# Kernel tuning notes

Hardware: AMD Instinct MI355X
Metric: run time of the kernel (lower is better)

## Reference

```python
import jax, jax.numpy as jnp
import numpy as np

B, S, H = 512, 200, 256

def setup_inputs() -> dict:
    key = jax.random.key(0)
    ks = jax.random.split(key, 7)
    scale = 1.0 / np.sqrt(H)
    return {
        "all_memory": jax.random.normal(ks[0], (B, S, H), dtype=jnp.float32),
        "last_memory": jax.random.normal(ks[1], (B, H), dtype=jnp.float32),
        "U": jax.random.normal(ks[2], (H, H), dtype=jnp.float32) * scale,   # U_meta weight
        "W": jax.random.normal(ks[3], (H, H), dtype=jnp.float32) * scale,   # W_meta weight
        "V": jax.random.normal(ks[4], (H, 1), dtype=jnp.float32) * scale,   # V_meta weight (stored as [H,1])
        "MetaW": jax.random.normal(ks[5], (4, H), dtype=jnp.float32) * scale,  # Meta weight
        "Metab": jax.random.normal(ks[6], (4,), dtype=jnp.float32) * scale,    # Meta bias ('multiple' mode)
    }

def reference(all_memory, last_memory, U, W, V, MetaW, Metab):
    # U_meta(all_memory): [B,S,H]; W_meta(last_memory): [B,H] broadcast over S
    a = jnp.einsum('bsh,kh->bsk', all_memory, U)
    l = jnp.einsum('bh,kh->bk', last_memory, W)
    # additive attention score: V_meta(tanh(a + l)) -> [B,S]
    scores = jnp.einsum('bsh,h->bs', jnp.tanh(a + l[:, None, :]), V[:, 0])
    alpha = jax.nn.softmax(scores, axis=1)  # softmax over seq dim
    pooled = jnp.einsum('bs,bsh->bh', alpha, all_memory)  # weighted sum of values
    return pooled @ MetaW.T + Metab  # [B, 4]
```

## Files before the change

### kernel.cpp

```cpp
#include <hip/hip_runtime.h>
#include <hip/hip_bf16.h>
#include <math.h>

#define NB 512
#define NS 200
#define NH 256
#define TILE_S 32
#define LDSPAD 8
#define LDW (NH + LDSPAD)
#define WS_STRIDE 258
#define NPART (NB * 2)

#define OFF_PART 0
#define OFF_L    (NPART * WS_STRIDE)
#define OFF_UB   (OFF_L + NB * NH)
#define WS_FLOATS_PRE  (OFF_UB + (NH * NH) / 2)

typedef _Float16 f16x8 __attribute__((ext_vector_type(8)));
typedef float    f32x4 __attribute__((ext_vector_type(4)));

__global__ __launch_bounds__(256)
void precompute(const float* __restrict__ lastm, const float* __restrict__ W,
                const float* __restrict__ U,
                float* __restrict__ l_ws, _Float16* __restrict__ Uswz)
{
  const int t = threadIdx.x;
  if (blockIdx.x < NB) {
    const int b = blockIdx.x;
    __shared__ float lm_sm[NH];
    lm_sm[t] = lastm[(size_t)b * NH + t];
    __syncthreads();
    const float4* wrow = (const float4*)(W + (size_t)t * NH);
    const float4* lrow = (const float4*)lm_sm;
    float a0 = 0.f, a1 = 0.f, a2 = 0.f, a3 = 0.f;
#pragma unroll 8
    for (int i = 0; i < NH / 4; ++i) {
      float4 w4 = wrow[i];
      float4 m4 = lrow[i];
      a0 = fmaf(w4.x, m4.x, a0);
      a1 = fmaf(w4.y, m4.y, a1);
      a2 = fmaf(w4.z, m4.z, a2);
      a3 = fmaf(w4.w, m4.w, a3);
    }
    l_ws[(size_t)b * NH + t] = (a0 + a1) + (a2 + a3);
  } else {
    const int id    = (blockIdx.x - NB) * 256 + t;
    const int n_blk = id >> 9;
    const int kk    = (id >> 6) & 7;
    const int lane  = id & 63;
    const int row   = n_blk * 16 + (lane & 15);
    const int col   = kk * 32 + (lane >> 4) * 8;
    const float4* s = (const float4*)(U + (size_t)row * NH + col);
    const float4 a = s[0], c = s[1];
    f16x8 pk;
    pk[0] = (_Float16)a.x; pk[1] = (_Float16)a.y;
    pk[2] = (_Float16)a.z; pk[3] = (_Float16)a.w;
    pk[4] = (_Float16)c.x; pk[5] = (_Float16)c.y;
    pk[6] = (_Float16)c.z; pk[7] = (_Float16)c.w;
    *(f16x8*)(Uswz + (size_t)id * 8) = pk;
  }
}

template<bool PRE>
__global__ __launch_bounds__(512, 4)
void fused_meta_attn_part(const float* __restrict__ mem,
                          const float* __restrict__ lastm,
                          const float* __restrict__ U,
                          const float* __restrict__ W,
                          const float* __restrict__ V,
                          const float* __restrict__ l_ws,
                          const _Float16* __restrict__ Uswz,
                          float* __restrict__ part)
{
  const int b    = blockIdx.x >> 1;
  const int half = blockIdx.x & 1;
  const int s_begin = half ? 96 : 0;
  const int s_end   = half ? NS : 96;
  const int ntiles  = half ? 4 : 3;

  const int t     = threadIdx.x;
  const int wave  = t >> 6;
  const int lane  = t & 63;
  const int m16   = lane & 15;
  const int quad  = lane >> 4;
  const int hcol  = t & 255;
  const int rhalf = t >> 8;

  __shared__ __align__(16) _Float16 hi_sm[TILE_S][LDW];
  __shared__ __align__(16) _Float16 lo_sm[TILE_S][LDW];
  __shared__ float swave_sm[8][TILE_S];
  __shared__ __align__(16) float e_sm[TILE_S];
  __shared__ float mz_sm[2];
  __shared__ float l_sm[NH];
  __shared__ float lm_sm[NH];

  if (!PRE) {
    if (t < NH) lm_sm[t] = lastm[(size_t)b * NH + t];
    __syncthreads();
    if (t < NH) {
      const float4* wrow = (const float4*)(W + (size_t)t * NH);
      const float4* lrow = (const float4*)lm_sm;
      float a0 = 0.f, a1 = 0.f, a2 = 0.f, a3 = 0.f;
#pragma unroll 8
      for (int i = 0; i < NH / 4; ++i) {
        float4 w4 = wrow[i];
        float4 m4 = lrow[i];
        a0 = fmaf(w4.x, m4.x, a0);
        a1 = fmaf(w4.y, m4.y, a1);
        a2 = fmaf(w4.z, m4.z, a2);
        a3 = fmaf(w4.w, m4.w, a3);
      }
      l_sm[t] = (a0 + a1) + (a2 + a3);
    }
    __syncthreads();
  }

  float l_reg[2], v_reg[2];
#pragma unroll
  for (int nf = 0; nf < 2; ++nf) {
    const int n = wave * 32 + nf * 16 + m16;
    l_reg[nf] = PRE ? l_ws[(size_t)b * NH + n] : l_sm[n];
    v_reg[nf] = V[n];
  }
  const float vsum  = v_reg[0] + v_reg[1];
  const float vm2_0 = -2.f * v_reg[0];
  const float vm2_1 = -2.f * v_reg[1];

  f16x8 u_frag[2][8];
  if (PRE) {
    const _Float16* uw = Uswz + ((size_t)(wave * 2 * 8 * 64) + lane) * 8;
#pragma unroll
    for (int nf = 0; nf < 2; ++nf)
#pragma unroll
      for (int kk = 0; kk < 8; ++kk)
        u_frag[nf][kk] = *(const f16x8*)(uw + (size_t)((nf * 8 + kk) << 9));
  } else {
#pragma unroll
    for (int nf = 0; nf < 2; ++nf) {
      const int n = wave * 32 + nf * 16 + m16;
      const float* urow = U + (size_t)n * NH;
#pragma unroll
      for (int kk = 0; kk < 8; ++kk) {
        const float4 lo = *(const float4*)(urow + kk * 32 + quad * 8);
        const float4 hi = *(const float4*)(urow + kk * 32 + quad * 8 + 4);
        f16x8 f;
        f[0] = (_Float16)lo.x; f[1] = (_Float16)lo.y;
        f[2] = (_Float16)lo.z; f[3] = (_Float16)lo.w;
        f[4] = (_Float16)hi.x; f[5] = (_Float16)hi.y;
        f[6] = (_Float16)hi.z; f[7] = (_Float16)hi.w;
        u_frag[nf][kk] = f;
      }
    }
  }

  float m_run  = -INFINITY;
  float Z      = 0.f;
  float pooled = 0.f;

  for (int tile = 0; tile < ntiles; ++tile) {
    const int s0   = s_begin + tile * TILE_S;
    const int rows = min(TILE_S, s_end - s0);

    const float4* src4 = (const float4*)(mem + ((size_t)b * NS + s0) * NH);
#pragma unroll
    for (int i = 0; i < 2; ++i) {
      const int f2  = i * 512 + t;
      const int row = f2 >> 5;
      const int c8  = (f2 & 31) * 8;
      f16x8 ph, pl;
      if (row < rows) {
        const float4 a = src4[f2 * 2];
        const float4 c = src4[f2 * 2 + 1];
#define CVT_HL(idx, val) { const float x_ = (val); const _Float16 h_ = (_Float16)x_; \
                           ph[idx] = h_; pl[idx] = (_Float16)(x_ - (float)h_); }
        CVT_HL(0, a.x) CVT_HL(1, a.y) CVT_HL(2, a.z) CVT_HL(3, a.w)
        CVT_HL(4, c.x) CVT_HL(5, c.y) CVT_HL(6, c.z) CVT_HL(7, c.w)
#undef CVT_HL
      } else {
        ph = (f16x8)(_Float16)0.f;
        pl = (f16x8)(_Float16)0.f;
      }
      *(f16x8*)&hi_sm[row][c8] = ph;
      *(f16x8*)&lo_sm[row][c8] = pl;
    }
    __syncthreads();

    f32x4 acc[2][2];
    const f32x4 fzero = {0.f, 0.f, 0.f, 0.f};
#pragma unroll
    for (int mt = 0; mt < 2; ++mt)
#pragma unroll
      for (int nf = 0; nf < 2; ++nf)
        acc[mt][nf] = fzero;

#pragma unroll
    for (int kk = 0; kk < 8; ++kk) {
      const int c = kk * 32 + quad * 8;
      f16x8 a0h = *(const f16x8*)&hi_sm[m16][c];
      f16x8 a1h = *(const f16x8*)&hi_sm[16 + m16][c];
      f16x8 a0l = *(const f16x8*)&lo_sm[m16][c];
      f16x8 a1l = *(const f16x8*)&lo_sm[16 + m16][c];
#pragma unroll
      for (int nf = 0; nf < 2; ++nf) {
        acc[0][nf] = __builtin_amdgcn_mfma_f32_16x16x32_f16(a0h, u_frag[nf][kk], acc[0][nf], 0, 0, 0);
        acc[1][nf] = __builtin_amdgcn_mfma_f32_16x16x32_f16(a1h, u_frag[nf][kk], acc[1][nf], 0, 0, 0);
        acc[0][nf] = __builtin_amdgcn_mfma_f32_16x16x32_f16(a0l, u_frag[nf][kk], acc[0][nf], 0, 0, 0);
        acc[1][nf] = __builtin_amdgcn_mfma_f32_16x16x32_f16(a1l, u_frag[nf][kk], acc[1][nf], 0, 0, 0);
      }
    }

    float p[2][4];
#pragma unroll
    for (int mt = 0; mt < 2; ++mt) {
#pragma unroll
      for (int reg = 0; reg < 4; ++reg) {
        const float x0 = acc[mt][0][reg] + l_reg[0];
        const float x1 = acc[mt][1][reg] + l_reg[1];
        const float e0 = __expf(x0 + x0);
        const float e1 = __expf(x1 + x1);
        float s = vsum;
        s += __fdividef(vm2_0, e0 + 1.f);
        s += __fdividef(vm2_1, e1 + 1.f);
        p[mt][reg] = s;
      }
    }
#pragma unroll
    for (int off = 1; off < 16; off <<= 1) {
#pragma unroll
      for (int mt = 0; mt < 2; ++mt)
#pragma unroll
        for (int reg = 0; reg < 4; ++reg)
          p[mt][reg] += __shfl_xor(p[mt][reg], off);
    }
    if (m16 == 0) {
#pragma unroll
      for (int mt = 0; mt < 2; ++mt)
#pragma unroll
        for (int reg = 0; reg < 4; ++reg)
          swave_sm[wave][mt * 16 + quad * 4 + reg] = p[mt][reg];
    }
    __syncthreads();

    if (t < TILE_S) {
      float s = swave_sm[0][t];
#pragma unroll
      for (int w = 1; w < 8; ++w) s += swave_sm[w][t];
      const float sv = (t < rows) ? s : -INFINITY;
      float mt_ = sv;
#pragma unroll
      for (int off = 1; off < 32; off <<= 1)
        mt_ = fmaxf(mt_, __shfl_xor(mt_, off));
      const float m_new = fmaxf(m_run, mt_);
      float e = (t < rows) ? __expf(sv - m_new) : 0.f;
      e_sm[t] = e;
      float z = e;
#pragma unroll
      for (int off = 1; off < 32; off <<= 1)
        z += __shfl_xor(z, off);
      if (t == 0) { mz_sm[0] = m_new; mz_sm[1] = z; }
    }
    __syncthreads();

    const float m_new = mz_sm[0];
    const float z_new = mz_sm[1];
    const float fac   = __expf(m_run - m_new);
    m_run = m_new;
    Z = fmaf(Z, fac, z_new);

    const int r0 = rhalf * 16;
    const float4 ev0 = *(const float4*)&e_sm[r0 + 0];
    const float4 ev1 = *(const float4*)&e_sm[r0 + 4];
    const float4 ev2 = *(const float4*)&e_sm[r0 + 8];
    const float4 ev3 = *(const float4*)&e_sm[r0 + 12];
    float pt = 0.f;
    pt = fmaf(ev0.x, (float)hi_sm[r0 +  0][hcol], pt);
    pt = fmaf(ev0.y, (float)hi_sm[r0 +  1][hcol], pt);
    pt = fmaf(ev0.z, (float)hi_sm[r0 +  2][hcol], pt);
    pt = fmaf(ev0.w, (float)hi_sm[r0 +  3][hcol], pt);
    pt = fmaf(ev1.x, (float)hi_sm[r0 +  4][hcol], pt);
    pt = fmaf(ev1.y, (float)hi_sm[r0 +  5][hcol], pt);
    pt = fmaf(ev1.z, (float)hi_sm[r0 +  6][hcol], pt);
    pt = fmaf(ev1.w, (float)hi_sm[r0 +  7][hcol], pt);
    pt = fmaf(ev2.x, (float)hi_sm[r0 +  8][hcol], pt);
    pt = fmaf(ev2.y, (float)hi_sm[r0 +  9][hcol], pt);
    pt = fmaf(ev2.z, (float)hi_sm[r0 + 10][hcol], pt);
    pt = fmaf(ev2.w, (float)hi_sm[r0 + 11][hcol], pt);
    pt = fmaf(ev3.x, (float)hi_sm[r0 + 12][hcol], pt);
    pt = fmaf(ev3.y, (float)hi_sm[r0 + 13][hcol], pt);
    pt = fmaf(ev3.z, (float)hi_sm[r0 + 14][hcol], pt);
    pt = fmaf(ev3.w, (float)hi_sm[r0 + 15][hcol], pt);
    pooled = fmaf(pooled, fac, pt);
    __syncthreads();
  }

  float* scratch = &swave_sm[0][0];
  if (rhalf == 1) scratch[hcol] = pooled;
  __syncthreads();
  float* base = part + (size_t)blockIdx.x * WS_STRIDE;
  if (t == 0) { base[0] = m_run; base[1] = Z; }
  if (rhalf == 0) base[2 + hcol] = pooled + scratch[hcol];
}

__global__ __launch_bounds__(256)
void merge_project(const float* __restrict__ part,
                   const float* __restrict__ MetaW,
                   const float* __restrict__ Metab,
                   float* __restrict__ out)
{
  const int b    = blockIdx.x;
  const int t    = threadIdx.x;
  const int wave = t >> 6;
  const int lane = t & 63;

  __shared__ float pooled_sm[NH];

  const float* b0 = part + (size_t)(b * 2)     * WS_STRIDE;
  const float* b1 = part + (size_t)(b * 2 + 1) * WS_STRIDE;
  const float m0 = b0[0], Z0 = b0[1];
  const float m1 = b1[0], Z1 = b1[1];
  const float mm = fmaxf(m0, m1);
  const float w0 = __expf(m0 - mm);
  const float w1 = __expf(m1 - mm);
  const float Zi = 1.f / (Z0 * w0 + Z1 * w1);

  pooled_sm[t] = (b0[2 + t] * w0 + b1[2 + t] * w1) * Zi;
  __syncthreads();

  float s = 0.f;
#pragma unroll
  for (int i = 0; i < 4; ++i) {
    const int h = i * 64 + lane;
    s = fmaf(pooled_sm[h], MetaW[(size_t)wave * NH + h], s);
  }
#pragma unroll
  for (int off = 32; off > 0; off >>= 1)
    s += __shfl_down(s, off);
  if (lane == 0)
    out[b * 4 + wave] = s + Metab[wave];
}

extern "C" void kernel_launch(void* const* d_in, const int* in_sizes, int n_in,
                              void* d_out, int out_size, void* d_ws, size_t ws_size,
                              hipStream_t stream) {
  const float* mem   = (const float*)d_in[0];
  const float* lastm = (const float*)d_in[1];
  const float* U     = (const float*)d_in[2];
  const float* W     = (const float*)d_in[3];
  const float* V     = (const float*)d_in[4];
  const float* MetaW = (const float*)d_in[5];
  const float* Metab = (const float*)d_in[6];
  float* out = (float*)d_out;
  float* ws  = (float*)d_ws;

  float* part = ws + OFF_PART;

  if (ws_size >= (size_t)WS_FLOATS_PRE * sizeof(float)) {
    float*    l_ws = ws + OFF_L;
    _Float16* Uswz = (_Float16*)(ws + OFF_UB);
    hipLaunchKernelGGL(precompute, dim3(NB + 32), dim3(256), 0, stream,
                       lastm, W, U, l_ws, Uswz);
    hipLaunchKernelGGL(fused_meta_attn_part<true>, dim3(NPART), dim3(512), 0, stream,
                       mem, lastm, U, W, V, l_ws, Uswz, part);
  } else {
    hipLaunchKernelGGL(fused_meta_attn_part<false>, dim3(NPART), dim3(512), 0, stream,
                       mem, lastm, U, W, V, (const float*)nullptr, (const _Float16*)nullptr, part);
  }
  hipLaunchKernelGGL(merge_project, dim3(NB), dim3(256), 0, stream,
                     part, MetaW, Metab, out);
}
```

Before: 210.8 us.

## Double-buffer memory tiles with register prefetch and use DPP row reductions

Stores the hi/lo fp16 memory tiles in two LDS buffers. The next tile is loaded from global into registers before the current tile's MFMA work and is converted and written to the other buffer during the softmax phase. This overlaps global loads with compute and removes one barrier per tile. It also swaps the shuffle-based 16-lane score reduction for DPP adds, and changes the pooled accumulation so each thread holds 8 columns over 2 rows, with a final 16-way LDS reduction. The larger LDS footprint may lower how many blocks fit per CU.

After: 246.7 us. 17.0% more time.

```diff
diff --git a/kernel.cpp b/kernel.cpp
--- a/kernel.cpp
+++ b/kernel.cpp
@@ -18,6 +18,19 @@
 
 typedef _Float16 f16x8 __attribute__((ext_vector_type(8)));
 typedef float    f32x4 __attribute__((ext_vector_type(4)));
+
+template<int CTRL>
+__device__ __forceinline__ float dpp_xadd(float v) {
+  return v + __int_as_float(
+      __builtin_amdgcn_update_dpp(0, __float_as_int(v), CTRL, 0xf, 0xf, true));
+}
+__device__ __forceinline__ float row16_sum(float v) {
+  v = dpp_xadd<0xB1>(v);
+  v = dpp_xadd<0x4E>(v);
+  v = dpp_xadd<0x124>(v);
+  v = dpp_xadd<0x128>(v);
+  return v;
+}
 
 __global__ __launch_bounds__(256)
 void precompute(const float* __restrict__ lastm, const float* __restrict__ W,
@@ -61,6 +74,9 @@
   }
 }
 
+#define CVT_HL(idx, val) { const float x_ = (val); const _Float16 h_ = (_Float16)x_; \
+                           ph[idx] = h_; pl[idx] = (_Float16)(x_ - (float)h_); }
+
 template<bool PRE>
 __global__ __launch_bounds__(512, 4)
 void fused_meta_attn_part(const float* __restrict__ mem,
@@ -83,18 +99,19 @@
   const int lane  = t & 63;
   const int m16   = lane & 15;
   const int quad  = lane >> 4;
-  const int hcol  = t & 255;
-  const int rhalf = t >> 8;
-
-  __shared__ __align__(16) _Float16 hi_sm[TILE_S][LDW];
-  __shared__ __align__(16) _Float16 lo_sm[TILE_S][LDW];
+  const int g     = t >> 5;
+  const int hblk  = (t & 31) * 8;
+
+  __shared__ __align__(16) _Float16 hi_sm[2][TILE_S][LDW];
+  __shared__ __align__(16) _Float16 lo_sm[2][TILE_S][LDW];
   __shared__ float swave_sm[8][TILE_S];
-  __shared__ __align__(16) float e_sm[TILE_S];
+  __shared__ float e_sm[TILE_S];
   __shared__ float mz_sm[2];
-  __shared__ float l_sm[NH];
-  __shared__ float lm_sm[NH];
-
-  if (!PRE) {
+
+  float l_reg[2], v_reg[2];
+  if constexpr (!PRE) {
+    __shared__ float l_sm[NH];
+    __shared__ float lm_sm[NH];
     if (t < NH) lm_sm[t] = lastm[(size_t)b * NH + t];
     __syncthreads();
     if (t < NH) {
@@ -113,21 +130,23 @@
       l_sm[t] = (a0 + a1) + (a2 + a3);
     }
     __syncthreads();
-  }
-
-  float l_reg[2], v_reg[2];
-#pragma unroll
-  for (int nf = 0; nf < 2; ++nf) {
-    const int n = wave * 32 + nf * 16 + m16;
-    l_reg[nf] = PRE ? l_ws[(size_t)b * NH + n] : l_sm[n];
-    v_reg[nf] = V[n];
-  }
+#pragma unroll
+    for (int nf = 0; nf < 2; ++nf)
+      l_reg[nf] = l_sm[wave * 32 + nf * 16 + m16];
+  } else {
+#pragma unroll
+    for (int nf = 0; nf < 2; ++nf)
+      l_reg[nf] = l_ws[(size_t)b * NH + wave * 32 + nf * 16 + m16];
+  }
+#pragma unroll
+  for (int nf = 0; nf < 2; ++nf)
+    v_reg[nf] = V[wave * 32 + nf * 16 + m16];
   const float vsum  = v_reg[0] + v_reg[1];
   const float vm2_0 = -2.f * v_reg[0];
   const float vm2_1 = -2.f * v_reg[1];
 
   f16x8 u_frag[2][8];
-  if (PRE) {
+  if constexpr (PRE) {
     const _Float16* uw = Uswz + ((size_t)(wave * 2 * 8 * 64) + lane) * 8;
 #pragma unroll
     for (int nf = 0; nf < 2; ++nf)
@@ -153,37 +172,49 @@
     }
   }
 
-  float m_run  = -INFINITY;
-  float Z      = 0.f;
-  float pooled = 0.f;
+  {
+    const float4* src4 = (const float4*)(mem + ((size_t)b * NS + s_begin) * NH);
+    const int f0 = t, f1 = 512 + t;
+    const float4 a0 = src4[f0 * 2], a1 = src4[f0 * 2 + 1];
+    const float4 b0 = src4[f1 * 2], b1 = src4[f1 * 2 + 1];
+    {
+      f16x8 ph, pl;
+      CVT_HL(0, a0.x) CVT_HL(1, a0.y) CVT_HL(2, a0.z) CVT_HL(3, a0.w)
+      CVT_HL(4, a1.x) CVT_HL(5, a1.y) CVT_HL(6, a1.z) CVT_HL(7, a1.w)
+      *(f16x8*)&hi_sm[0][f0 >> 5][(f0 & 31) * 8] = ph;
+      *(f16x8*)&lo_sm[0][f0 >> 5][(f0 & 31) * 8] = pl;
+    }
+    {
+      f16x8 ph, pl;
+      CVT_HL(0, b0.x) CVT_HL(1, b0.y) CVT_HL(2, b0.z) CVT_HL(3, b0.w)
+      CVT_HL(4, b1.x) CVT_HL(5, b1.y) CVT_HL(6, b1.z) CVT_HL(7, b1.w)
+      *(f16x8*)&hi_sm[0][f1 >> 5][(f1 & 31) * 8] = ph;
+      *(f16x8*)&lo_sm[0][f1 >> 5][(f1 & 31) * 8] = pl;
+    }
+  }
+  __syncthreads();
+
+  float m_run = -INFINITY;
+  float Z     = 0.f;
+  float pooledv[8];
+#pragma unroll
+  for (int j = 0; j < 8; ++j) pooledv[j] = 0.f;
 
   for (int tile = 0; tile < ntiles; ++tile) {
-    const int s0   = s_begin + tile * TILE_S;
+    const int cur = tile & 1;
+    const int nxt = cur ^ 1;
+    const int s0  = s_begin + tile * TILE_S;
     const int rows = min(TILE_S, s_end - s0);
-
-    const float4* src4 = (const float4*)(mem + ((size_t)b * NS + s0) * NH);
-#pragma unroll
-    for (int i = 0; i < 2; ++i) {
-      const int f2  = i * 512 + t;
-      const int row = f2 >> 5;
-      const int c8  = (f2 & 31) * 8;
-      f16x8 ph, pl;
-      if (row < rows) {
-        const float4 a = src4[f2 * 2];
-        const float4 c = src4[f2 * 2 + 1];
-#define CVT_HL(idx, val) { const float x_ = (val); const _Float16 h_ = (_Float16)x_; \
-                           ph[idx] = h_; pl[idx] = (_Float16)(x_ - (float)h_); }
-        CVT_HL(0, a.x) CVT_HL(1, a.y) CVT_HL(2, a.z) CVT_HL(3, a.w)
-        CVT_HL(4, c.x) CVT_HL(5, c.y) CVT_HL(6, c.z) CVT_HL(7, c.w)
-#undef CVT_HL
-      } else {
-        ph = (f16x8)(_Float16)0.f;
-        pl = (f16x8)(_Float16)0.f;
-      }
-      *(f16x8*)&hi_sm[row][c8] = ph;
-      *(f16x8*)&lo_sm[row][c8] = pl;
-    }
-    __syncthreads();
+    const int rows_next = (tile + 1 < ntiles) ? min(TILE_S, s_end - (s0 + TILE_S)) : 0;
+
+    float4 p00, p01, p10, p11;
+    const bool ld0 = (t >> 5) < rows_next;
+    const bool ld1 = ((512 + t) >> 5) < rows_next;
+    {
+      const float4* nsrc = (const float4*)(mem + ((size_t)b * NS + s0 + TILE_S) * NH);
+      if (ld0) { p00 = nsrc[t * 2];         p01 = nsrc[t * 2 + 1]; }
+      if (ld1) { p10 = nsrc[(512 + t) * 2]; p11 = nsrc[(512 + t) * 2 + 1]; }
+    }
 
     f32x4 acc[2][2];
     const f32x4 fzero = {0.f, 0.f, 0.f, 0.f};
@@ -196,10 +227,10 @@
 #pragma unroll
     for (int kk = 0; kk < 8; ++kk) {
       const int c = kk * 32 + quad * 8;
-      f16x8 a0h = *(const f16x8*)&hi_sm[m16][c];
-      f16x8 a1h = *(const f16x8*)&hi_sm[16 + m16][c];
-      f16x8 a0l = *(const f16x8*)&lo_sm[m16][c];
-      f16x8 a1l = *(const f16x8*)&lo_sm[16 + m16][c];
+      f16x8 a0h = *(const f16x8*)&hi_sm[cur][m16][c];
+      f16x8 a1h = *(const f16x8*)&hi_sm[cur][16 + m16][c];
+      f16x8 a0l = *(const f16x8*)&lo_sm[cur][m16][c];
+      f16x8 a1l = *(const f16x8*)&lo_sm[cur][16 + m16][c];
 #pragma unroll
       for (int nf = 0; nf < 2; ++nf) {
         acc[0][nf] = __builtin_amdgcn_mfma_f32_16x16x32_f16(a0h, u_frag[nf][kk], acc[0][nf], 0, 0, 0);
@@ -209,7 +240,6 @@
       }
     }
 
-    float p[2][4];
 #pragma unroll
     for (int mt = 0; mt < 2; ++mt) {
 #pragma unroll
@@ -221,23 +251,10 @@
         float s = vsum;
         s += __fdividef(vm2_0, e0 + 1.f);
         s += __fdividef(vm2_1, e1 + 1.f);
-        p[mt][reg] = s;
+        s = row16_sum(s);
+        if (m16 == 0)
+          swave_sm[wave][mt * 16 + quad * 4 + reg] = s;
       }
-    }
-#pragma unroll
-    for (int off = 1; off < 16; off <<= 1) {
-#pragma unroll
-      for (int mt = 0; mt < 2; ++mt)
-#pragma unroll
-        for (int reg = 0; reg < 4; ++reg)
-          p[mt][reg] += __shfl_xor(p[mt][reg], off);
-    }
-    if (m16 == 0) {
-#pragma unroll
-      for (int mt = 0; mt < 2; ++mt)
-#pragma unroll
-        for (int reg = 0; reg < 4; ++reg)
-          swave_sm[wave][mt * 16 + quad * 4 + reg] = p[mt][reg];
     }
     __syncthreads();
 
@@ -259,6 +276,21 @@
         z += __shfl_xor(z, off);
       if (t == 0) { mz_sm[0] = m_new; mz_sm[1] = z; }
     }
+
+    if (ld0) {
+      f16x8 ph, pl;
+      CVT_HL(0, p00.x) CVT_HL(1, p00.y) CVT_HL(2, p00.z) CVT_HL(3, p00.w)
+      CVT_HL(4, p01.x) CVT_HL(5, p01.y) CVT_HL(6, p01.z) CVT_HL(7, p01.w)
+      *(f16x8*)&hi_sm[nxt][t >> 5][(t & 31) * 8] = ph;
+      *(f16x8*)&lo_sm[nxt][t >> 5][(t & 31) * 8] = pl;
+    }
+    if (ld1) {
+      f16x8 ph, pl;
+      CVT_HL(0, p10.x) CVT_HL(1, p10.y) CVT_HL(2, p10.z) CVT_HL(3, p10.w)
+      CVT_HL(4, p11.x) CVT_HL(5, p11.y) CVT_HL(6, p11.z) CVT_HL(7, p11.w)
+      *(f16x8*)&hi_sm[nxt][(512 + t) >> 5][(t & 31) * 8] = ph;
+      *(f16x8*)&lo_sm[nxt][(512 + t) >> 5][(t & 31) * 8] = pl;
+    }
     __syncthreads();
 
     const float m_new = mz_sm[0];
@@ -267,38 +299,33 @@
     m_run = m_new;
     Z = fmaf(Z, fac, z_new);
 
-    const int r0 = rhalf * 16;
-    const float4 ev0 = *(const float4*)&e_sm[r0 + 0];
-    const float4 ev1 = *(const float4*)&e_sm[r0 + 4];
-    const float4 ev2 = *(const float4*)&e_sm[r0 + 8];
-    const float4 ev3 = *(const float4*)&e_sm[r0 + 12];
-    float pt = 0.f;
-    pt = fmaf(ev0.x, (float)hi_sm[r0 +  0][hcol], pt);
-    pt = fmaf(ev0.y, (float)hi_sm[r0 +  1][hcol], pt);
-    pt = fmaf(ev0.z, (float)hi_sm[r0 +  2][hcol], pt);
-    pt = fmaf(ev0.w, (float)hi_sm[r0 +  3][hcol], pt);
-    pt = fmaf(ev1.x, (float)hi_sm[r0 +  4][hcol], pt);
-    pt = fmaf(ev1.y, (float)hi_sm[r0 +  5][hcol], pt);
-    pt = fmaf(ev1.z, (float)hi_sm[r0 +  6][hcol], pt);
-    pt = fmaf(ev1.w, (float)hi_sm[r0 +  7][hcol], pt);
-    pt = fmaf(ev2.x, (float)hi_sm[r0 +  8][hcol], pt);
-    pt = fmaf(ev2.y, (float)hi_sm[r0 +  9][hcol], pt);
-    pt = fmaf(ev2.z, (float)hi_sm[r0 + 10][hcol], pt);
-    pt = fmaf(ev2.w, (float)hi_sm[r0 + 11][hcol], pt);
-    pt = fmaf(ev3.x, (float)hi_sm[r0 + 12][hcol], pt);
-    pt = fmaf(ev3.y, (float)hi_sm[r0 + 13][hcol], pt);
-    pt = fmaf(ev3.z, (float)hi_sm[r0 + 14][hcol], pt);
-    pt = fmaf(ev3.w, (float)hi_sm[r0 + 15][hcol], pt);
-    pooled = fmaf(pooled, fac, pt);
-    __syncthreads();
-  }
-
-  float* scratch = &swave_sm[0][0];
-  if (rhalf == 1) scratch[hcol] = pooled;
+    const float e0 = e_sm[2 * g];
+    const float e1 = e_sm[2 * g + 1];
+    const f16x8 r0 = *(const f16x8*)&hi_sm[cur][2 * g][hblk];
+    const f16x8 r1 = *(const f16x8*)&hi_sm[cur][2 * g + 1][hblk];
+#pragma unroll
+    for (int j = 0; j < 8; ++j)
+      pooledv[j] = fmaf(e0, (float)r0[j], fmaf(e1, (float)r1[j], pooledv[j] * fac));
+    __syncthreads();
+  }
+
+  float* scratch = (float*)&hi_sm[0][0][0];
+  {
+    f32x4 lo4 = {pooledv[0], pooledv[1], pooledv[2], pooledv[3]};
+    f32x4 hi4 = {pooledv[4], pooledv[5], pooledv[6], pooledv[7]};
+    *(f32x4*)&scratch[g * 264 + hblk]     = lo4;
+    *(f32x4*)&scratch[g * 264 + hblk + 4] = hi4;
+  }
   __syncthreads();
   float* base = part + (size_t)blockIdx.x * WS_STRIDE;
   if (t == 0) { base[0] = m_run; base[1] = Z; }
-  if (rhalf == 0) base[2 + hcol] = pooled + scratch[hcol];
+  if (t < NH) {
+    float s = 0.f;
+#pragma unroll
+    for (int r = 0; r < 16; ++r)
+      s += scratch[r * 264 + t];
+    base[2 + t] = s;
+  }
 }
 
 __global__ __launch_bounds__(256)
```
